# Optimization experiments

Hardware: AMD Instinct MI355X
Metric: run time of the kernel (lower is better)

## Reference

```python
import jax, jax.numpy as jnp
import numpy as np

N, D, E, EDGE_DIM, HID4 = 8192, 128, 262144, 50, 32


def setup_inputs() -> dict:
    key = jax.random.key(0)
    k = jax.random.split(key, 8)
    return {
        "mag": jax.random.uniform(k[0], (N, D), dtype=jnp.float32),
        "phase": jax.random.normal(k[1], (N, D), dtype=jnp.float32),
        "edge_index": jax.random.randint(k[2], (2, E), 0, N, dtype=jnp.int64),
        "rbf": jax.random.uniform(k[3], (E, EDGE_DIM), dtype=jnp.float32),
        "W1": jax.random.normal(k[4], (EDGE_DIM, HID4), dtype=jnp.float32) * 0.1,
        "b1": jnp.zeros((HID4,), dtype=jnp.float32),
        "W2": jax.random.normal(k[5], (HID4, 1), dtype=jnp.float32) * 0.1,
        "b2": jnp.zeros((1,), dtype=jnp.float32),
    }


def reference(mag, phase, edge_index, rbf, W1, b1, W2, b2):
    # score_ij = sum_d |z_i||z_j| cos(theta_i - theta_j) / sqrt(D)
    # cos(a-b) identity: = (mag*cos(phase)) @ (mag*cos(phase))^T + (mag*sin)@(mag*sin)^T
    scale = jnp.sqrt(jnp.asarray(mag.shape[-1], mag.dtype))
    a = mag * jnp.cos(phase)  # [N, D]
    b = mag * jnp.sin(phase)  # [N, D]
    scores = (a @ a.T + b @ b.T) / scale  # [N, N]
    # edge bias: Linear -> SiLU -> Linear -> scalar, scattered onto (i, j)
    h = jax.nn.silu(rbf @ W1 + b1)       # [E, HID4]
    bias = (h @ W2 + b2)[:, 0]           # [E]
    scores = scores.at[edge_index[0], edge_index[1]].add(bias)
    attn = jax.nn.softmax(scores, axis=1)  # softmax over keys j
    new_mag = attn @ mag
    new_phase = attn @ phase
    return new_mag, new_phase
```

## Files before the change

### kernel.cpp

```cpp
#include <hip/hip_runtime.h>
#include <hip/hip_bf16.h>

#define NN 8192
#define DD 128
#define DQK 256
#define EE 262144
#define EDGE_DIM 50
#define HID 32
#define CAP 96
#define SCALE 0.08838834764831845f
#define SCALE_LOG2E 0.12752455522410585f

using f32x4 = __attribute__((ext_vector_type(4))) float;
using f32x2 = __attribute__((ext_vector_type(2))) float;
using bf16x8 = __attribute__((ext_vector_type(8))) short;
using s16x4 = __attribute__((ext_vector_type(4))) short;

static __device__ __forceinline__ short f2b(float f) {
  __hip_bfloat16 h = __float2bfloat16(f);
  return __builtin_bit_cast(short, h);
}
static __device__ __forceinline__ float b2f(short s) {
  unsigned u = ((unsigned)(unsigned short)s) << 16;
  return __builtin_bit_cast(float, u);
}
static __device__ __forceinline__ void gll(const short* g, short* l) {
  __builtin_amdgcn_global_load_lds(
      (const __attribute__((address_space(1))) void*)g,
      (__attribute__((address_space(3))) void*)l, 16, 0, 0);
}

__global__ __launch_bounds__(256) void k1_mega(
    const float* __restrict__ mag, const float* __restrict__ phase,
    short* __restrict__ qkb, short* __restrict__ vtb, short* __restrict__ vb16,
    const float* __restrict__ rbf, const float* __restrict__ W1,
    const float* __restrict__ b1, const float* __restrict__ W2,
    const float* __restrict__ b2, const int* __restrict__ eidx,
    float* __restrict__ bias, int* __restrict__ cnt, int* __restrict__ slot) {
  __shared__ float tile[64][65];
  int b = blockIdx.x;
  int tid = threadIdx.x;
  if (b < 4096) {
    int t = b * 256 + tid;
    int n = t >> 7, d = t & 127;
    float m = mag[t], p = phase[t];
    float sn, cs;
    __sincosf(p, &sn, &cs);
    qkb[(size_t)n * DQK + d] = f2b(m * cs);
    qkb[(size_t)n * DQK + 128 + d] = f2b(m * sn);
    vb16[(size_t)n * DQK + d] = f2b(m);
    vb16[(size_t)n * DQK + 128 + d] = f2b(p);
    return;
  }
  if (b < 4608) {
    int r = b - 4096;
    int bn = r & 127, bd = (r >> 7) & 1, sel = r >> 8;
    const float* src = sel ? phase : mag;
#pragma unroll
    for (int rep = 0; rep < 16; ++rep) {
      int idx = rep * 256 + tid;
      int rr = idx >> 6, c = idx & 63;
      tile[rr][c] = src[(size_t)(bn * 64 + rr) * DD + bd * 64 + c];
    }
    __syncthreads();
#pragma unroll
    for (int rep = 0; rep < 16; ++rep) {
      int idx = rep * 256 + tid;
      int rr = idx >> 6, c = idx & 63;
      vtb[(size_t)(sel * 128 + bd * 64 + rr) * NN + bn * 64 + c] = f2b(tile[c][rr]);
    }
    return;
  }
  int e = (b - 4608) * 256 + tid;
  const float* rrow = rbf + (size_t)e * EDGE_DIM;
  f32x4 r4[12];
#pragma unroll
  for (int k = 0; k < 12; ++k) r4[k] = *reinterpret_cast<const f32x4*>(rrow + 4 * k);
  f32x2 rt2 = *reinterpret_cast<const f32x2*>(rrow + 48);
  float h[HID];
#pragma unroll
  for (int jj = 0; jj < HID; ++jj) h[jj] = b1[jj];
#pragma unroll
  for (int k = 0; k < 48; ++k) {
    float r = r4[k >> 2][k & 3];
#pragma unroll
    for (int jj = 0; jj < HID; ++jj) h[jj] += r * W1[k * HID + jj];
  }
#pragma unroll
  for (int jj = 0; jj < HID; ++jj)
    h[jj] += rt2.x * W1[48 * HID + jj] + rt2.y * W1[49 * HID + jj];
  float outv = b2[0];
#pragma unroll
  for (int jj = 0; jj < HID; ++jj) {
    float x = h[jj];
    outv += W2[jj] * (x / (1.0f + __expf(-x)));
  }
  bias[e] = outv;
  int i = eidx[e];
  int p = atomicAdd(&cnt[i], 1);
  if (p < CAP) slot[i * CAP + p] = e;
}

__global__ __launch_bounds__(64) void k2_merge(
    const int* __restrict__ eidx, const float* __restrict__ bias,
    const int* __restrict__ cntArr, const int* __restrict__ slot,
    unsigned* __restrict__ edgeJB, int* __restrict__ qoff) {
  __shared__ int js[CAP];
  __shared__ float bsv[CAP];
  __shared__ float bsum_s[CAP];
  __shared__ unsigned char keepf[CAP];
  int i = blockIdx.x;
  int lane = threadIdx.x;
  int cnt = cntArr[i];
  if (cnt > CAP) cnt = CAP;
  for (int p = lane; p < cnt; p += 64) {
    int e = slot[i * CAP + p];
    js[p] = eidx[EE + e];
    bsv[p] = bias[e];
  }
  __syncthreads();
  for (int p = lane; p < cnt; p += 64) {
    int j = js[p];
    float bsum = bsv[p];
    int kp = 1;
    for (int qq = 0; qq < cnt; ++qq) {
      if (qq == p || js[qq] != j) continue;
      if (qq < p) { kp = 0; break; }
      bsum += bsv[qq];
    }
    keepf[p] = (unsigned char)kp;
    bsum_s[p] = bsum;
  }
  __syncthreads();
  for (int p = lane; p < cnt; p += 64) {
    if (!keepf[p]) continue;
    int j = js[p];
    int r = 0;
    for (int qq = 0; qq < cnt; ++qq) r += (keepf[qq] && js[qq] < j);
    edgeJB[(size_t)i * CAP + r] =
        (((unsigned)j) << 16) | (unsigned short)f2b(__expf(bsum_s[p]));
  }
  if (lane < 5) {
    int bound = lane * 2048;
    int c = 0;
    for (int qq = 0; qq < cnt; ++qq) c += (keepf[qq] && js[qq] < bound);
    qoff[i * 5 + lane] = c;
  }
}

constexpr int TBM = 64;
constexpr int TBN = 128;

template <int NSPLIT>
__global__ __launch_bounds__(512, 4) void k5_flash(
    const short* __restrict__ qk,
    const short* __restrict__ vt,
    const unsigned* __restrict__ ejb,
    const int* __restrict__ qoff,
    float* __restrict__ nump,
    float* __restrict__ denp) {
  constexpr int QCOLS = NN / NSPLIT;
  constexpr int NCHUNK = QCOLS / TBN;
  constexpr int GPQ = 8 / NSPLIT;
  __shared__ alignas(16) short Qs[TBM * 256];
  __shared__ alignas(16) short KV[2 * TBN * 64];
  __shared__ alignas(16) short Ps[TBM * 128];
  int b = blockIdx.x;
  int q = (b & 7) / GPQ;
  int rb = (b >> 3) * GPQ + (b & (GPQ - 1));
  int tid = threadIdx.x;
  int w = tid >> 6, lane = tid & 63;
  int wr = w >> 2, wc = w & 3;
  int l15 = lane & 15, quad = lane >> 4;
  int rsw = l15 & 7;
  int wbase = w * 64;
  int r0 = rb * TBM;
  int cbase = q * QCOLS;

#pragma unroll
  for (int p = 0; p < 4; ++p) {
    int idx = p * 512 + tid;
    int row = idx >> 5, gs = idx & 31;
    gll(qk + (size_t)(r0 + row) * DQK + ((gs ^ (row & 7)) * 8),
        &Qs[(p * 512 + wbase) * 8]);
  }

  const unsigned* erow = ejb + (size_t)(r0 + (tid & 63)) * CAP;
  int cursor = 0, cend = 0;
  unsigned nextE = 0xFFFFFFFFu;
  if (tid < TBM) {
    int qb = cbase >> 11;
    cursor = qoff[(r0 + tid) * 5 + qb];
    cend = qoff[(r0 + tid) * 5 + qb + (QCOLS >> 11)];
    if (cursor < cend) nextE = erow[cursor];
  }
  float denAcc = 0.f;

  f32x4 o[2][4] = {};
  float den[2] = {0.f, 0.f};
  __syncthreads();

  for (int ch = 0; ch < NCHUNK; ++ch) {
    int c0 = cbase + ch * TBN;
#pragma unroll
    for (int p = 0; p < 2; ++p) {
      int idx = p * 512 + tid;
      int col = idx >> 3, gs = idx & 7;
      gll(qk + (size_t)(c0 + col) * DQK + ((gs ^ (col & 7)) * 8),
          &KV[(p * 512 + wbase) * 8]);
    }
    __syncthreads();
    f32x4 s[2][2] = {};
#pragma unroll
    for (int bk = 0; bk < 4; ++bk) {
      int buf = bk & 1;
      if (bk < 3) {
        int nb = buf ^ 1;
#pragma unroll
        for (int p = 0; p < 2; ++p) {
          int idx = p * 512 + tid;
          int col = idx >> 3, gs = idx & 7;
          gll(qk + (size_t)(c0 + col) * DQK + (bk + 1) * 64 + ((gs ^ (col & 7)) * 8),
              &KV[nb * 8192 + (p * 512 + wbase) * 8]);
        }
      }
#pragma unroll
      for (int ks = 0; ks < 2; ++ks) {
        int g = ks * 4 + quad;
        bf16x8 a[2], bb[2];
#pragma unroll
        for (int rt = 0; rt < 2; ++rt)
          a[rt] = *(const bf16x8*)&Qs[(wr * 32 + rt * 16 + l15) * 256 +
                                      ((bk * 8 + g) ^ rsw) * 8];
#pragma unroll
        for (int ct = 0; ct < 2; ++ct)
          bb[ct] = *(const bf16x8*)&KV[buf * 8192 + (wc * 32 + ct * 16 + l15) * 64 +
                                       (g ^ rsw) * 8];
#pragma unroll
        for (int rt = 0; rt < 2; ++rt)
#pragma unroll
          for (int ct = 0; ct < 2; ++ct)
            s[ct][rt] = __builtin_amdgcn_mfma_f32_16x16x32_bf16(bb[ct], a[rt],
                                                                s[ct][rt], 0, 0, 0);
      }
      __syncthreads();
    }
#pragma unroll
    for (int p = 0; p < 4; ++p) {
      int idx = p * 512 + tid;
      int feat = idx >> 3, gs = idx & 7;
      gll(vt + (size_t)feat * NN + c0 + ((gs ^ (feat & 7)) * 8),
          &KV[(p * 512 + wbase) * 8]);
    }
#pragma unroll
    for (int rt = 0; rt < 2; ++rt) {
      int row = wr * 32 + rt * 16 + l15;
#pragma unroll
      for (int ct = 0; ct < 2; ++ct) {
        s16x4 pk;
#pragma unroll
        for (int r = 0; r < 4; ++r) {
          float pv = exp2f(s[ct][rt][r] * SCALE_LOG2E);
          den[rt] += pv;
          pk[r] = f2b(pv);
        }
        int cg = wc * 4 + ct * 2 + (quad >> 1);
        *reinterpret_cast<s16x4*>(
            &Ps[row * 128 + ((cg ^ (row & 7)) * 8 + (quad & 1) * 4)]) = pk;
      }
    }
    __syncthreads();
    if (tid < TBM) {
      unsigned limit = (unsigned)(c0 + TBN);
      while ((nextE >> 16) < limit) {
        unsigned dj = (nextE >> 16) - (unsigned)c0;
        float eb = b2f((short)(nextE & 0xFFFFu));
        short* ps = &Ps[tid * 128 + (((dj >> 3) ^ (tid & 7)) * 8 + (int)(dj & 7))];
        float oldp = b2f(*ps);
        *ps = f2b(oldp * eb);
        denAcc += oldp * (eb - 1.0f);
        ++cursor;
        nextE = (cursor < cend) ? erow[cursor] : 0xFFFFFFFFu;
      }
    }
    __syncthreads();
#pragma unroll
    for (int jb = 0; jb < 2; ++jb) {
      if (jb == 1) {
        __syncthreads();
#pragma unroll
        for (int p = 0; p < 4; ++p) {
          int idx = p * 512 + tid;
          int feat = idx >> 3, gs = idx & 7;
          gll(vt + (size_t)feat * NN + c0 + 64 + ((gs ^ (feat & 7)) * 8),
              &KV[(p * 512 + wbase) * 8]);
        }
        __syncthreads();
      }
#pragma unroll
      for (int ks = 0; ks < 2; ++ks) {
        int g = ks * 4 + quad;
        bf16x8 pa[2], vb[4];
#pragma unroll
        for (int rt = 0; rt < 2; ++rt) {
          int row = wr * 32 + rt * 16 + l15;
          pa[rt] = *(const bf16x8*)&Ps[row * 128 +
                                       (((jb * 8 + g) ^ (row & 7)) * 8)];
        }
#pragma unroll
        for (int ft = 0; ft < 4; ++ft)
          vb[ft] = *(const bf16x8*)&KV[(wc * 64 + ft * 16 + l15) * 64 + (g ^ rsw) * 8];
#pragma unroll
        for (int rt = 0; rt < 2; ++rt)
#pragma unroll
          for (int ft = 0; ft < 4; ++ft)
            o[rt][ft] = __builtin_amdgcn_mfma_f32_16x16x32_bf16(pa[rt], vb[ft],
                                                                o[rt][ft], 0, 0, 0);
      }
    }
    __syncthreads();
  }
  float* npB = nump + (size_t)q * NN * DQK;
#pragma unroll
  for (int rt = 0; rt < 2; ++rt)
#pragma unroll
    for (int ft = 0; ft < 4; ++ft) {
      int row = r0 + wr * 32 + rt * 16 + quad * 4;
      int feat = wc * 64 + ft * 16 + l15;
#pragma unroll
      for (int r = 0; r < 4; ++r)
        npB[(size_t)(row + r) * DQK + feat] = o[rt][ft][r];
    }
  float* dl = reinterpret_cast<float*>(KV);
#pragma unroll
  for (int rt = 0; rt < 2; ++rt) {
    float d = den[rt];
    d += __shfl_xor(d, 16);
    d += __shfl_xor(d, 32);
    if (lane < 16) dl[wc * TBM + wr * 32 + rt * 16 + lane] = d;
  }
  __syncthreads();
  if (tid < TBM) {
    float d = dl[0 * TBM + tid] + dl[1 * TBM + tid] + dl[2 * TBM + tid] +
              dl[3 * TBM + tid] + denAcc;
    denp[q * NN + r0 + tid] = d;
  }
}

__global__ __launch_bounds__(64) void k6_norm(
    const float* __restrict__ nump, const float* __restrict__ denp,
    float* __restrict__ out, int nsplit) {
  int i = blockIdx.x;
  int lane = threadIdx.x;
  f32x4 a = {0.f, 0.f, 0.f, 0.f};
  float den = 0.f;
  for (int qq = 0; qq < nsplit; ++qq) {
    a += *reinterpret_cast<const f32x4*>(nump + ((size_t)qq * NN + i) * DQK + lane * 4);
    den += denp[qq * NN + i];
  }
  float inv = 1.0f / den;
  a *= inv;
  float* dst = (lane < 32) ? (out + (size_t)i * DD + lane * 4)
                           : (out + (size_t)NN * DD + (size_t)i * DD + lane * 4 - 128);
  *reinterpret_cast<f32x4*>(dst) = a;
}

constexpr size_t OFF_QK = 0;
constexpr size_t OFF_VT = (size_t)NN * DQK * 2;
constexpr size_t OFF_VB16 = OFF_VT + (size_t)DQK * NN * 2;
constexpr size_t OFF_BIAS = OFF_VB16 + (size_t)NN * DQK * 2;
constexpr size_t OFF_CNT = OFF_BIAS + (size_t)EE * 4;
constexpr size_t OFF_SLOT = OFF_CNT + (size_t)NN * 4;
constexpr size_t OFF_EJB = (OFF_SLOT + (size_t)NN * CAP * 4 + 255) & ~(size_t)255;
constexpr size_t OFF_QOFF = OFF_EJB + (size_t)NN * CAP * 4;
constexpr size_t OFF_NUMP = (OFF_QOFF + (size_t)NN * 5 * 4 + 255) & ~(size_t)255;
constexpr size_t WS_NEED4 = OFF_NUMP + 4ull * NN * DQK * 4 + 4ull * NN * 4;
constexpr size_t WS_NEED2 = OFF_NUMP + 2ull * NN * DQK * 4 + 2ull * NN * 4;

extern "C" void kernel_launch(void* const* d_in, const int* in_sizes, int n_in,
                              void* d_out, int out_size, void* d_ws, size_t ws_size,
                              hipStream_t stream) {
  const float* mag = (const float*)d_in[0];
  const float* phase = (const float*)d_in[1];
  const int* eidx = (const int*)d_in[2];
  const float* rbf = (const float*)d_in[3];
  const float* W1 = (const float*)d_in[4];
  const float* b1 = (const float*)d_in[5];
  const float* W2 = (const float*)d_in[6];
  const float* b2 = (const float*)d_in[7];
  float* out = (float*)d_out;
  char* ws = (char*)d_ws;
  if (ws_size < WS_NEED2) return;
  int nsplit = (ws_size >= WS_NEED4) ? 4 : 2;

  short* qkb = (short*)(ws + OFF_QK);
  short* vtb = (short*)(ws + OFF_VT);
  short* vb16 = (short*)(ws + OFF_VB16);
  float* bias = (float*)(ws + OFF_BIAS);
  int* cnt = (int*)(ws + OFF_CNT);
  int* slot = (int*)(ws + OFF_SLOT);
  unsigned* edgeJB = (unsigned*)(ws + OFF_EJB);
  int* qoff = (int*)(ws + OFF_QOFF);
  float* nump = (float*)(ws + OFF_NUMP);
  float* denp = (float*)(ws + OFF_NUMP + (size_t)nsplit * NN * DQK * 4);

  hipMemsetAsync(cnt, 0, (size_t)NN * 4, stream);
  k1_mega<<<5632, 256, 0, stream>>>(mag, phase, qkb, vtb, vb16, rbf, W1, b1, W2,
                                    b2, eidx, bias, cnt, slot);
  k2_merge<<<NN, 64, 0, stream>>>(eidx, bias, cnt, slot, edgeJB, qoff);
  if (nsplit == 4)
    k5_flash<4><<<(NN / TBM) * 4, 512, 0, stream>>>(qkb, vtb, edgeJB, qoff, nump, denp);
  else
    k5_flash<2><<<(NN / TBM) * 2, 512, 0, stream>>>(qkb, vtb, edgeJB, qoff, nump, denp);
  k6_norm<<<NN, 64, 0, stream>>>(nump, denp, out, nsplit);
}
```

Baseline: 259.6 us.

## Parallelize sparse edge-bias application across 8 threads per row with per-chunk offsets

The merge kernel now writes a prefix-count offset for every 128-column chunk (65 per row) instead of 5 coarse ones. In the flash kernel, all 512 threads apply the edge bias as 8 threads per row, each striding over that chunk's edges, instead of 64 threads walking serial cursors. The first edge entry is prefetched before the QK compute to hide its global-load latency, and the per-row denominator corrections are reduced by shuffles at the end. This removes a serialized, divergent loop between two barriers, at the cost of more offset storage and extra offset loads per chunk.

```diff
diff --git a/kernel.cpp b/kernel.cpp
--- a/kernel.cpp
+++ b/kernel.cpp
@@ -104,7 +104,7 @@
 __global__ __launch_bounds__(64) void k2_merge(
     const int* __restrict__ eidx, const float* __restrict__ bias,
     const int* __restrict__ cntArr, const int* __restrict__ slot,
-    unsigned* __restrict__ edgeJB, int* __restrict__ qoff) {
+    unsigned* __restrict__ edgeJB, int* __restrict__ qoffc) {
   __shared__ int js[CAP];
   __shared__ float bsv[CAP];
   __shared__ float bsum_s[CAP];
@@ -140,11 +140,11 @@
     edgeJB[(size_t)i * CAP + r] =
         (((unsigned)j) << 16) | (unsigned short)f2b(__expf(bsum_s[p]));
   }
-  if (lane < 5) {
-    int bound = lane * 2048;
+  for (int k = lane; k <= 64; k += 64) {
+    int bound = k * 128;
     int c = 0;
     for (int qq = 0; qq < cnt; ++qq) c += (keepf[qq] && js[qq] < bound);
-    qoff[i * 5 + lane] = c;
+    qoffc[i * 65 + k] = c;
   }
 }
 
@@ -156,7 +156,7 @@
     const short* __restrict__ qk,
     const short* __restrict__ vt,
     const unsigned* __restrict__ ejb,
-    const int* __restrict__ qoff,
+    const int* __restrict__ qoffc,
     float* __restrict__ nump,
     float* __restrict__ denp) {
   constexpr int QCOLS = NN / NSPLIT;
@@ -176,6 +176,10 @@
   int wbase = w * 64;
   int r0 = rb * TBM;
   int cbase = q * QCOLS;
+  int row8 = tid >> 3, sl0 = tid & 7;
+  const unsigned* erow = ejb + (size_t)(r0 + row8) * CAP;
+  const int* qrow = qoffc + (size_t)(r0 + row8) * 65 + (cbase >> 7);
+  float denAcc = 0.f;
 
 #pragma unroll
   for (int p = 0; p < 4; ++p) {
@@ -185,17 +189,6 @@
         &Qs[(p * 512 + wbase) * 8]);
   }
 
-  const unsigned* erow = ejb + (size_t)(r0 + (tid & 63)) * CAP;
-  int cursor = 0, cend = 0;
-  unsigned nextE = 0xFFFFFFFFu;
-  if (tid < TBM) {
-    int qb = cbase >> 11;
-    cursor = qoff[(r0 + tid) * 5 + qb];
-    cend = qoff[(r0 + tid) * 5 + qb + (QCOLS >> 11)];
-    if (cursor < cend) nextE = erow[cursor];
-  }
-  float denAcc = 0.f;
-
   f32x4 o[2][4] = {};
   float den[2] = {0.f, 0.f};
   __syncthreads();
@@ -209,6 +202,8 @@
       gll(qk + (size_t)(c0 + col) * DQK + ((gs ^ (col & 7)) * 8),
           &KV[(p * 512 + wbase) * 8]);
     }
+    int es = qrow[ch], ee = qrow[ch + 1];
+    unsigned entPre = (es + sl0 < ee) ? erow[es + sl0] : 0u;
     __syncthreads();
     f32x4 s[2][2] = {};
 #pragma unroll
@@ -270,18 +265,22 @@
       }
     }
     __syncthreads();
-    if (tid < TBM) {
-      unsigned limit = (unsigned)(c0 + TBN);
-      while ((nextE >> 16) < limit) {
-        unsigned dj = (nextE >> 16) - (unsigned)c0;
-        float eb = b2f((short)(nextE & 0xFFFFu));
-        short* ps = &Ps[tid * 128 + (((dj >> 3) ^ (tid & 7)) * 8 + (int)(dj & 7))];
-        float oldp = b2f(*ps);
-        *ps = f2b(oldp * eb);
-        denAcc += oldp * (eb - 1.0f);
-        ++cursor;
-        nextE = (cursor < cend) ? erow[cursor] : 0xFFFFFFFFu;
-      }
+    if (es + sl0 < ee) {
+      unsigned dj = (entPre >> 16) - (unsigned)c0;
+      float eb = b2f((short)(entPre & 0xFFFFu));
+      short* ps = &Ps[row8 * 128 + (((dj >> 3) ^ (row8 & 7)) * 8 + (int)(dj & 7))];
+      float oldp = b2f(*ps);
+      *ps = f2b(oldp * eb);
+      denAcc += oldp * (eb - 1.0f);
+    }
+    for (int t = es + 8 + sl0; t < ee; t += 8) {
+      unsigned ent = erow[t];
+      unsigned dj = (ent >> 16) - (unsigned)c0;
+      float eb = b2f((short)(ent & 0xFFFFu));
+      short* ps = &Ps[row8 * 128 + (((dj >> 3) ^ (row8 & 7)) * 8 + (int)(dj & 7))];
+      float oldp = b2f(*ps);
+      *ps = f2b(oldp * eb);
+      denAcc += oldp * (eb - 1.0f);
     }
     __syncthreads();
 #pragma unroll
@@ -332,6 +331,7 @@
         npB[(size_t)(row + r) * DQK + feat] = o[rt][ft][r];
     }
   float* dl = reinterpret_cast<float*>(KV);
+  float* corr = reinterpret_cast<float*>(KV) + 4 * TBM;
 #pragma unroll
   for (int rt = 0; rt < 2; ++rt) {
     float d = den[rt];
@@ -339,10 +339,14 @@
     d += __shfl_xor(d, 32);
     if (lane < 16) dl[wc * TBM + wr * 32 + rt * 16 + lane] = d;
   }
+  denAcc += __shfl_xor(denAcc, 1);
+  denAcc += __shfl_xor(denAcc, 2);
+  denAcc += __shfl_xor(denAcc, 4);
+  if (sl0 == 0) corr[row8] = denAcc;
   __syncthreads();
   if (tid < TBM) {
     float d = dl[0 * TBM + tid] + dl[1 * TBM + tid] + dl[2 * TBM + tid] +
-              dl[3 * TBM + tid] + denAcc;
+              dl[3 * TBM + tid] + corr[tid];
     denp[q * NN + r0 + tid] = d;
   }
 }
@@ -373,7 +377,7 @@
 constexpr size_t OFF_SLOT = OFF_CNT + (size_t)NN * 4;
 constexpr size_t OFF_EJB = (OFF_SLOT + (size_t)NN * CAP * 4 + 255) & ~(size_t)255;
 constexpr size_t OFF_QOFF = OFF_EJB + (size_t)NN * CAP * 4;
-constexpr size_t OFF_NUMP = (OFF_QOFF + (size_t)NN * 5 * 4 + 255) & ~(size_t)255;
+constexpr size_t OFF_NUMP = (OFF_QOFF + (size_t)NN * 65 * 4 + 255) & ~(size_t)255;
 constexpr size_t WS_NEED4 = OFF_NUMP + 4ull * NN * DQK * 4 + 4ull * NN * 4;
 constexpr size_t WS_NEED2 = OFF_NUMP + 2ull * NN * DQK * 4 + 2ull * NN * 4;
 
@@ -400,17 +404,17 @@
   int* cnt = (int*)(ws + OFF_CNT);
   int* slot = (int*)(ws + OFF_SLOT);
   unsigned* edgeJB = (unsigned*)(ws + OFF_EJB);
-  int* qoff = (int*)(ws + OFF_QOFF);
+  int* qoffc = (int*)(ws + OFF_QOFF);
   float* nump = (float*)(ws + OFF_NUMP);
   float* denp = (float*)(ws + OFF_NUMP + (size_t)nsplit * NN * DQK * 4);
 
   hipMemsetAsync(cnt, 0, (size_t)NN * 4, stream);
   k1_mega<<<5632, 256, 0, stream>>>(mag, phase, qkb, vtb, vb16, rbf, W1, b1, W2,
                                     b2, eidx, bias, cnt, slot);
-  k2_merge<<<NN, 64, 0, stream>>>(eidx, bias, cnt, slot, edgeJB, qoff);
+  k2_merge<<<NN, 64, 0, stream>>>(eidx, bias, cnt, slot, edgeJB, qoffc);
   if (nsplit == 4)
-    k5_flash<4><<<(NN / TBM) * 4, 512, 0, stream>>>(qkb, vtb, edgeJB, qoff, nump, denp);
+    k5_flash<4><<<(NN / TBM) * 4, 512, 0, stream>>>(qkb, vtb, edgeJB, qoffc, nump, denp);
   else
-    k5_flash<2><<<(NN / TBM) * 2, 512, 0, stream>>>(qkb, vtb, edgeJB, qoff, nump, denp);
+    k5_flash<2><<<(NN / TBM) * 2, 512, 0, stream>>>(qkb, vtb, edgeJB, qoffc, nump, denp);
   k6_norm<<<NN, 64, 0, stream>>>(nump, denp, out, nsplit);
 }
```

New measurement: 264.4 us. About the same (+1.9%).
